# Performance work log

Measured on AMD Instinct MI355X. Metric: run time of the kernel, lower is better.

The kernel has to match this reference:

```python
import jax, jax.numpy as jnp
import numpy as np

B, D, N = 131072, 512, 1


def setup_inputs() -> dict:
    key = jax.random.key(0)
    k1, k2, k3 = jax.random.split(key, 3)
    return {
        "global_img": jax.random.normal(k1, (B, D, N), dtype=jnp.float32),
        "global_pos": jax.random.normal(k2, (B, D, N), dtype=jnp.float32),
        "global_neg": jax.random.normal(k3, (B, D, N), dtype=jnp.float32),
    }


def reference(global_img, global_pos, global_neg):
    b, d, n = global_img.shape  # n must be 1 for the views below (as in torch)
    temperature = 50.0
    eps = 1e-8  # F.cosine_similarity eps

    query = global_img
    # cosine similarity along the feature dim (axis=1) -> [B, N]
    num = jnp.sum(global_pos * query, axis=1)
    denom = (jnp.maximum(jnp.linalg.norm(global_pos, axis=1), eps)
             * jnp.maximum(jnp.linalg.norm(query, axis=1), eps))
    dist = num / denom
    max_i = jnp.argmax(dist, axis=1)  # [B] indices into N (all 0 when N==1)

    # batched gather of the best positive column per sample: [B, D, 1]
    batch_pos = jnp.take_along_axis(global_pos, max_i[:, None, None], axis=2)

    # bmm(query.view(B,1,D), batch_pos.view(B,D,1)) -> per-sample dot product [B,1,1]
    q = query.reshape(b, 1, d)
    dot_pos = jnp.einsum('bod,bdo->b', q, batch_pos.reshape(b, d, 1))[:, None, None]
    exp_pos = jnp.exp(dot_pos / temperature)

    dot_neg = jnp.einsum('bod,bdo->b', q, global_neg.reshape(b, d, 1))[:, None, None]
    exp_neg = jnp.exp(dot_neg / temperature)
    sum_neg = jnp.sum(exp_neg, axis=2, keepdims=True)  # [B,1,1]

    global_loss = -jnp.log(exp_pos / (exp_pos + sum_neg))
    return jnp.mean(global_loss)
```

## Files before the change

kernel.cpp:

```cpp
#include <hip/hip_runtime.h>


#define BLOCK 256
#define WAVES_PER_BLOCK (BLOCK / 64)
#define NBLOCKS 2048
#define DCOLS 512

__global__ __launch_bounds__(BLOCK) void gcl_partial_kernel(
    const float* __restrict__ img,
    const float* __restrict__ pos,
    const float* __restrict__ neg,
    float* __restrict__ partials,
    int B)
{
    const int lane  = threadIdx.x & 63;
    const int wave  = threadIdx.x >> 6;
    const int gwave = blockIdx.x * WAVES_PER_BLOCK + wave;
    const int nwaves = gridDim.x * WAVES_PER_BLOCK;

    float acc = 0.0f;

    for (int row = gwave; row < B; row += nwaves) {
        const size_t base = (size_t)row * DCOLS;
        const float4* i4 = (const float4*)(img + base);
        const float4* p4 = (const float4*)(pos + base);
        const float4* n4 = (const float4*)(neg + base);

        float4 a0 = i4[lane];
        float4 a1 = i4[lane + 64];
        float4 b0 = p4[lane];
        float4 b1 = p4[lane + 64];
        float4 c0 = n4[lane];
        float4 c1 = n4[lane + 64];

        float dp = a0.x * b0.x + a0.y * b0.y + a0.z * b0.z + a0.w * b0.w
                 + a1.x * b1.x + a1.y * b1.y + a1.z * b1.z + a1.w * b1.w;
        float dn = a0.x * c0.x + a0.y * c0.y + a0.z * c0.z + a0.w * c0.w
                 + a1.x * c1.x + a1.y * c1.y + a1.z * c1.z + a1.w * c1.w;

        #pragma unroll
        for (int off = 32; off >= 1; off >>= 1) {
            dp += __shfl_xor(dp, off, 64);
            dn += __shfl_xor(dn, off, 64);
        }

        if (lane == 0) {
            acc += log1pf(__expf((dn - dp) * 0.02f));
        }
    }

    __shared__ float sacc[WAVES_PER_BLOCK];
    if (lane == 0) sacc[wave] = acc;
    __syncthreads();

    if (threadIdx.x == 0) {
        float s = 0.0f;
        #pragma unroll
        for (int w = 0; w < WAVES_PER_BLOCK; ++w) s += sacc[w];
        partials[blockIdx.x] = s;
    }
}

__global__ __launch_bounds__(256) void gcl_final_kernel(
    const float* __restrict__ partials, int n, float* __restrict__ out, float invB)
{
    __shared__ float s[256];
    float a = 0.0f;
    for (int i = threadIdx.x; i < n; i += 256) a += partials[i];
    s[threadIdx.x] = a;
    __syncthreads();
    #pragma unroll
    for (int stride = 128; stride > 0; stride >>= 1) {
        if (threadIdx.x < stride) s[threadIdx.x] += s[threadIdx.x + stride];
        __syncthreads();
    }
    if (threadIdx.x == 0) out[0] = s[0] * invB;
}

extern "C" void kernel_launch(void* const* d_in, const int* in_sizes, int n_in,
                              void* d_out, int out_size, void* d_ws, size_t ws_size,
                              hipStream_t stream) {
    const float* img = (const float*)d_in[0];
    const float* pos = (const float*)d_in[1];
    const float* neg = (const float*)d_in[2];
    float* out = (float*)d_out;
    float* partials = (float*)d_ws;

    const int B = in_sizes[0] / DCOLS;

    int nblocks = NBLOCKS;
    if (ws_size < (size_t)nblocks * sizeof(float)) {
        nblocks = (int)(ws_size / sizeof(float));
        if (nblocks < 1) nblocks = 1;
    }

    gcl_partial_kernel<<<nblocks, BLOCK, 0, stream>>>(img, pos, neg, partials, B);
    gcl_final_kernel<<<1, 256, 0, stream>>>(partials, nblocks, out, 1.0f / (float)B);
}
```

Before: 645.9 us.

## Process four rows per wave with 16-lane groups and more loads in flight

Each wave now splits into four 16-lane groups, each handling one row and issuing eight float4 loads per input tensor instead of two. The aim is to raise memory-level parallelism per lane and shorten the cross-lane shuffle reduction. Per-lane accumulators are reduced across the wave once at the end. The cost is higher register use and tail handling through clamped row indices.

```diff
diff --git a/kernel.cpp b/kernel.cpp
--- a/kernel.cpp
+++ b/kernel.cpp
@@ -5,6 +5,10 @@
 #define WAVES_PER_BLOCK (BLOCK / 64)
 #define NBLOCKS 2048
 #define DCOLS 512
+#define F4_PER_ROW (DCOLS / 4)
+#define LANES_PER_ROW 16
+#define ROWS_PER_WAVE (64 / LANES_PER_ROW)
+#define K_STEPS (F4_PER_ROW / LANES_PER_ROW)
 
 __global__ __launch_bounds__(BLOCK) void gcl_partial_kernel(
     const float* __restrict__ img,
@@ -15,39 +19,54 @@
 {
     const int lane  = threadIdx.x & 63;
     const int wave  = threadIdx.x >> 6;
+    const int j     = lane & (LANES_PER_ROW - 1);
+    const int g     = lane >> 4;
     const int gwave = blockIdx.x * WAVES_PER_BLOCK + wave;
     const int nwaves = gridDim.x * WAVES_PER_BLOCK;
 
     float acc = 0.0f;
 
-    for (int row = gwave; row < B; row += nwaves) {
-        const size_t base = (size_t)row * DCOLS;
-        const float4* i4 = (const float4*)(img + base);
-        const float4* p4 = (const float4*)(pos + base);
-        const float4* n4 = (const float4*)(neg + base);
+    for (int rbase = gwave * ROWS_PER_WAVE; rbase < B; rbase += nwaves * ROWS_PER_WAVE) {
+        int row = rbase + g;
+        int row_c = row < B ? row : (B - 1);
 
-        float4 a0 = i4[lane];
-        float4 a1 = i4[lane + 64];
-        float4 b0 = p4[lane];
-        float4 b1 = p4[lane + 64];
-        float4 c0 = n4[lane];
-        float4 c1 = n4[lane + 64];
+        const size_t base = (size_t)row_c * F4_PER_ROW + j;
+        const float4* i4 = (const float4*)img + base;
+        const float4* p4 = (const float4*)pos + base;
+        const float4* n4 = (const float4*)neg + base;
 
-        float dp = a0.x * b0.x + a0.y * b0.y + a0.z * b0.z + a0.w * b0.w
-                 + a1.x * b1.x + a1.y * b1.y + a1.z * b1.z + a1.w * b1.w;
-        float dn = a0.x * c0.x + a0.y * c0.y + a0.z * c0.z + a0.w * c0.w
-                 + a1.x * c1.x + a1.y * c1.y + a1.z * c1.z + a1.w * c1.w;
+        float4 a[K_STEPS], b[K_STEPS], c[K_STEPS];
+        #pragma unroll
+        for (int k = 0; k < K_STEPS; ++k) {
+            a[k] = i4[(size_t)k * LANES_PER_ROW];
+            b[k] = p4[(size_t)k * LANES_PER_ROW];
+            c[k] = n4[(size_t)k * LANES_PER_ROW];
+        }
+
+        float dp0 = 0.0f, dp1 = 0.0f, dn0 = 0.0f, dn1 = 0.0f;
+        #pragma unroll
+        for (int k = 0; k < K_STEPS; k += 2) {
+            dp0 += a[k].x * b[k].x + a[k].y * b[k].y + a[k].z * b[k].z + a[k].w * b[k].w;
+            dn0 += a[k].x * c[k].x + a[k].y * c[k].y + a[k].z * c[k].z + a[k].w * c[k].w;
+            dp1 += a[k+1].x * b[k+1].x + a[k+1].y * b[k+1].y + a[k+1].z * b[k+1].z + a[k+1].w * b[k+1].w;
+            dn1 += a[k+1].x * c[k+1].x + a[k+1].y * c[k+1].y + a[k+1].z * c[k+1].z + a[k+1].w * c[k+1].w;
+        }
+        float dp = dp0 + dp1;
+        float dn = dn0 + dn1;
 
         #pragma unroll
-        for (int off = 32; off >= 1; off >>= 1) {
+        for (int off = 8; off >= 1; off >>= 1) {
             dp += __shfl_xor(dp, off, 64);
             dn += __shfl_xor(dn, off, 64);
         }
 
-        if (lane == 0) {
+        if (j == 0 && row < B) {
             acc += log1pf(__expf((dn - dp) * 0.02f));
         }
     }
+
+    #pragma unroll
+    for (int off = 32; off >= 1; off >>= 1) acc += __shfl_xor(acc, off, 64);
 
     __shared__ float sacc[WAVES_PER_BLOCK];
     if (lane == 0) sacc[wave] = acc;
```

Result: no change. 657.2 us (+1.8%).
